# Performance work log

Hardware: AMD Instinct MI355X
Metric: run time of the kernel (lower is better)

Reference implementation:

```python
import jax, jax.numpy as jnp
import numpy as np

B, T, INPUT_DIM = 4, 2048, 1024
DIM, H = 64, 16  # per-head dim, n_heads


def setup_inputs() -> dict:
    key = jax.random.key(0)
    k1, k2, k3, k4 = jax.random.split(key, 4)
    x = jax.random.normal(k1, (B, T, INPUT_DIM), dtype=jnp.float32)
    # nn.Linear(input_dim, 3*h*d, bias=False)
    w_qkv = jax.random.normal(k2, (INPUT_DIM, 3 * H * DIM), dtype=jnp.float32) * (INPUT_DIM ** -0.5)
    # nn.Linear(h*d, input_dim) with bias
    w_out = jax.random.normal(k3, (H * DIM, INPUT_DIM), dtype=jnp.float32) * ((H * DIM) ** -0.5)
    b_out = jax.random.normal(k4, (INPUT_DIM,), dtype=jnp.float32) * 0.01
    return {"x": x, "w_qkv": w_qkv, "w_out": w_out, "b_out": b_out}


def reference(x, w_qkv, w_out, b_out):
    b, t, _ = x.shape
    scale = DIM ** -0.5
    qkv = x @ w_qkv                                   # [b, t, 3*h*d]
    # 'b t (qkv h d) -> qkv b h t d'
    qkv = qkv.reshape(b, t, 3, H, DIM)
    qkv = jnp.transpose(qkv, (2, 0, 3, 1, 4))         # [3, b, h, t, d]
    q, k, v = qkv[0], qkv[1], qkv[2]
    dot = jnp.einsum('bhtd,bhkd->bhtk', q, k) * scale # [b, h, t, t]
    att = jax.nn.softmax(dot, axis=-1)
    out = jnp.einsum('bhtk,bhkd->bhtd', att, v)       # [b, h, t, d]
    out = jnp.transpose(out, (0, 2, 1, 3)).reshape(b, t, H * DIM)
    return out @ w_out + b_out
```

## Files before the change

### kernel.cpp

```cpp
#include <hip/hip_runtime.h>
#include <hip/hip_bf16.h>
#include <stdint.h>

typedef __attribute__((ext_vector_type(8))) short bf16x8;
typedef __attribute__((ext_vector_type(4))) short s16x4;
typedef __attribute__((ext_vector_type(4))) float f32x4;

__device__ __forceinline__ void mfma_bf16(f32x4& c, bf16x8 a, bf16x8 b) {
  asm("v_mfma_f32_16x16x32_bf16 %0, %1, %2, %0" : "+v"(c) : "v"(a), "v"(b));
}

__device__ __forceinline__ void gload_lds16(const void* g, void* lds) {
  __builtin_amdgcn_global_load_lds(
      (const __attribute__((address_space(1))) void*)g,
      (__attribute__((address_space(3))) void*)lds, 16, 0, 0);
}

__global__ void cvt_f32_bf16(const float* __restrict__ in, __hip_bfloat16* __restrict__ out, int n4) {
  int i = blockIdx.x * blockDim.x + threadIdx.x;
  if (i >= n4) return;
  float4 v = reinterpret_cast<const float4*>(in)[i];
  __hip_bfloat162 a = __float22bfloat162_rn(make_float2(v.x, v.y));
  __hip_bfloat162 b = __float22bfloat162_rn(make_float2(v.z, v.w));
  reinterpret_cast<__hip_bfloat162*>(out)[i * 2]     = a;
  reinterpret_cast<__hip_bfloat162*>(out)[i * 2 + 1] = b;
}

__global__ void transpose_cvt(const float* __restrict__ in, __hip_bfloat16* __restrict__ out,
                              int R, int C) {
  __shared__ float tile[32][33];
  int c0 = blockIdx.x * 32, r0 = blockIdx.y * 32;
#pragma unroll
  for (int k = 0; k < 4; k++)
    tile[threadIdx.y + 8 * k][threadIdx.x] =
        in[(size_t)(r0 + threadIdx.y + 8 * k) * C + c0 + threadIdx.x];
  __syncthreads();
#pragma unroll
  for (int k = 0; k < 4; k++)
    out[(size_t)(c0 + threadIdx.y + 8 * k) * R + r0 + threadIdx.x] =
        __float2bfloat16(tile[threadIdx.x][threadIdx.y + 8 * k]);
}

template <int MODE>
__global__ __launch_bounds__(256) void gemm_bf16(
    const __hip_bfloat16* __restrict__ A, const __hip_bfloat16* __restrict__ Bt,
    int M, int N, int K,
    __hip_bfloat16* __restrict__ qb, __hip_bfloat16* __restrict__ kb,
    __hip_bfloat16* __restrict__ vt,
    float* __restrict__ outp, const float* __restrict__ bias) {
  constexpr int BK = 32;
  __shared__ __align__(16) __hip_bfloat16 As[128 * BK];
  __shared__ __align__(16) __hip_bfloat16 Bs[128 * BK];
  const int tid = threadIdx.x;
  const int wave = tid >> 6, lane = tid & 63;
  const int wr = wave >> 1, wc = wave & 1;
  const int m0 = blockIdx.y * 128;
  const int n0 = (MODE == 2 ? 2048 : 0) + blockIdx.x * 128;

  f32x4 acc[4][4];
#pragma unroll
  for (int i = 0; i < 4; i++)
#pragma unroll
    for (int j = 0; j < 4; j++) acc[i][j] = (f32x4)(0.0f);

  const int c0 = wave * 2, c1 = c0 + 1;
  const int srow0 = c0 * 16 + (lane >> 2);
  const int srow1 = c1 * 16 + (lane >> 2);
  const int scol = (lane & 3) * 8;
  const __hip_bfloat16* Ag0 = A + (size_t)(m0 + srow0) * K + scol;
  const __hip_bfloat16* Ag1 = A + (size_t)(m0 + srow1) * K + scol;
  const __hip_bfloat16* Bg0 = Bt + (size_t)(n0 + srow0) * K + scol;
  const __hip_bfloat16* Bg1 = Bt + (size_t)(n0 + srow1) * K + scol;
  __hip_bfloat16* AsP0 = &As[c0 * 512];
  __hip_bfloat16* AsP1 = &As[c1 * 512];
  __hip_bfloat16* BsP0 = &Bs[c0 * 512];
  __hip_bfloat16* BsP1 = &Bs[c1 * 512];

  for (int kk = 0; kk < K; kk += BK) {
    gload_lds16(Ag0 + kk, AsP0);
    gload_lds16(Ag1 + kk, AsP1);
    gload_lds16(Bg0 + kk, BsP0);
    gload_lds16(Bg1 + kk, BsP1);
    __syncthreads();
    bf16x8 af[4], bfr[4];
#pragma unroll
    for (int i = 0; i < 4; i++)
      af[i] = *(const bf16x8*)&As[(wr * 64 + i * 16 + (lane & 15)) * BK + (lane >> 4) * 8];
#pragma unroll
    for (int j = 0; j < 4; j++)
      bfr[j] = *(const bf16x8*)&Bs[(wc * 64 + j * 16 + (lane & 15)) * BK + (lane >> 4) * 8];
#pragma unroll
    for (int i = 0; i < 4; i++)
#pragma unroll
      for (int j = 0; j < 4; j++) {
        if constexpr (MODE == 2)
          mfma_bf16(acc[i][j], bfr[j], af[i]);
        else
          mfma_bf16(acc[i][j], af[i], bfr[j]);
      }
    __syncthreads();
  }

  if constexpr (MODE == 0) {
#pragma unroll
    for (int j = 0; j < 4; j++) {
      int col = n0 + wc * 64 + j * 16 + (lane & 15);
      int sel = col >> 10;
      int h = (col >> 6) & 15;
      int d = col & 63;
      __hip_bfloat16* dst = sel ? kb : qb;
      float scl = sel ? 1.0f : 0.18033688f;
#pragma unroll
      for (int i = 0; i < 4; i++) {
#pragma unroll
        for (int r = 0; r < 4; r++) {
          int row = m0 + wr * 64 + i * 16 + (lane >> 4) * 4 + r;
          int b = row >> 11, t = row & 2047;
          dst[(((size_t)b * 16 + h) * 2048 + t) * 64 + d] = __float2bfloat16(acc[i][j][r] * scl);
        }
      }
    }
  } else if constexpr (MODE == 2) {
#pragma unroll
    for (int j = 0; j < 4; j++) {
#pragma unroll
      for (int r = 0; r < 4; r++) {
        int nrow = n0 + wc * 64 + j * 16 + (lane >> 4) * 4 + r;
        int h = (nrow >> 6) & 15;
        int d = nrow & 63;
#pragma unroll
        for (int i = 0; i < 4; i++) {
          int tcol = m0 + wr * 64 + i * 16 + (lane & 15);
          int b = tcol >> 11, t = tcol & 2047;
          vt[(((size_t)b * 16 + h) * 64 + d) * 2048 + t] = __float2bfloat16(acc[i][j][r]);
        }
      }
    }
  } else {
#pragma unroll
    for (int j = 0; j < 4; j++) {
      int col = n0 + wc * 64 + j * 16 + (lane & 15);
      float bv = bias[col];
#pragma unroll
      for (int i = 0; i < 4; i++) {
#pragma unroll
        for (int r = 0; r < 4; r++) {
          int row = m0 + wr * 64 + i * 16 + (lane >> 4) * 4 + r;
          outp[(size_t)row * N + col] = acc[i][j][r] + bv;
        }
      }
    }
  }
}

__global__ __launch_bounds__(256) void attn_fwd(
    const __hip_bfloat16* __restrict__ Qb, const __hip_bfloat16* __restrict__ Kb,
    const __hip_bfloat16* __restrict__ Vtg, __hip_bfloat16* __restrict__ Ob) {
  constexpr int T = 2048;
  constexpr float THR = 11.5f;
  __shared__ __align__(16) __hip_bfloat16 Ks[2][4096];
  __shared__ __align__(16) __hip_bfloat16 Vs[2][4096];
  __shared__ __align__(16) __hip_bfloat16 Ps[4][1024];
  const int tid = threadIdx.x, wave = tid >> 6, lane = tid & 63;

  int id = ((int)blockIdx.x & 7) * 256 + ((int)blockIdx.x >> 3);
  const int bh = id >> 5, q0 = (id & 31) * 64;
  const size_t baseQ = (size_t)bh * T * 64;
  const size_t baseV = (size_t)bh * 64 * T;

  bf16x8 qf[2];
  {
    const int qrow = q0 + wave * 16 + (lane & 15);
#pragma unroll
    for (int ks = 0; ks < 2; ks++)
      qf[ks] = *(const bf16x8*)&Qb[baseQ + (size_t)qrow * 64 + ks * 32 + (lane >> 4) * 8];
  }

  float m_run = -3.0e38f;
  float l_part = 0.0f;
  f32x4 o[4];
#pragma unroll
  for (int fd = 0; fd < 4; fd++) o[fd] = (f32x4)(0.0f);

  const int sr = lane >> 3;
  const int q8 = (lane & 7) ^ sr;
  const char* KgB = (const char*)(Kb + baseQ);
  const char* VgB = (const char*)(Vtg + baseV);
  const int cc0 = wave * 2, cc1 = cc0 + 1;
  char* PwB = (char*)&Ps[wave][0];
  const int prow = lane & 15, hi = lane >> 4;

#define STAGE(kt, buf)                                                                   \
  do {                                                                                   \
    char* kd = (char*)Ks[buf];                                                           \
    char* vd = (char*)Vs[buf];                                                           \
    gload_lds16(KgB + (size_t)((kt) * 64 + cc0 * 8 + sr) * 128 + q8 * 16, kd + cc0 * 1024); \
    gload_lds16(KgB + (size_t)((kt) * 64 + cc1 * 8 + sr) * 128 + q8 * 16, kd + cc1 * 1024); \
    gload_lds16(VgB + (size_t)(cc0 * 8 + sr) * 4096 + (kt) * 128 + q8 * 16, vd + cc0 * 1024); \
    gload_lds16(VgB + (size_t)(cc1 * 8 + sr) * 4096 + (kt) * 128 + q8 * 16, vd + cc1 * 1024); \
  } while (0)

  STAGE(0, 0);
  int cur = 0;

  for (int kt = 0; kt < T / 64; kt++) {
    if (kt < T / 64 - 1) {
      STAGE(kt + 1, cur ^ 1);
      asm volatile("s_waitcnt vmcnt(4)" ::: "memory");
    } else {
      asm volatile("s_waitcnt vmcnt(0)" ::: "memory");
    }
    __builtin_amdgcn_s_barrier();
    __builtin_amdgcn_sched_barrier(0);
    const char* KsB = (const char*)Ks[cur];
    const char* VtB = (const char*)Vs[cur];

    f32x4 s[4];
#pragma unroll
    for (int kf = 0; kf < 4; kf++) s[kf] = (f32x4)(0.0f);
    __builtin_amdgcn_s_setprio(1);
#pragma unroll
    for (int ks = 0; ks < 2; ks++) {
#pragma unroll
      for (int kf = 0; kf < 4; kf++) {
        int key = kf * 16 + prow;
        int byteoff = (key * 128 + ks * 64 + hi * 16) ^ ((key & 7) << 4);
        bf16x8 kfrag = *(const bf16x8*)(KsB + byteoff);
        mfma_bf16(s[kf], kfrag, qf[ks]);
      }
    }
    __builtin_amdgcn_s_setprio(0);

    float t0 = fmaxf(fmaxf(s[0][0], s[0][1]), s[0][2]);
    float t1 = fmaxf(fmaxf(s[0][3], s[1][0]), s[1][1]);
    float t2 = fmaxf(fmaxf(s[1][2], s[1][3]), s[2][0]);
    float t3 = fmaxf(fmaxf(s[2][1], s[2][2]), s[2][3]);
    float t4 = fmaxf(fmaxf(s[3][0], s[3][1]), s[3][2]);
    float tm = fmaxf(fmaxf(fmaxf(t0, t1), t2), fmaxf(fmaxf(t3, t4), s[3][3]));
    tm = fmaxf(tm, __shfl_xor(tm, 16));
    tm = fmaxf(tm, __shfl_xor(tm, 32));

    if (!__all(tm - m_run <= THR)) {
      float mn = fmaxf(m_run, tm);
      float alpha = __builtin_exp2f(m_run - mn);
      m_run = mn;
      l_part *= alpha;
#pragma unroll
      for (int r = 0; r < 4; r++) {
        float ar = __shfl(alpha, hi * 4 + r);
#pragma unroll
        for (int fd = 0; fd < 4; fd++) o[fd][r] *= ar;
      }
    }

    float rs0 = 0.0f, rs1 = 0.0f;
#pragma unroll
    for (int kf = 0; kf < 4; kf++) {
      float p0 = __builtin_exp2f(s[kf][0] - m_run);
      float p1 = __builtin_exp2f(s[kf][1] - m_run);
      float p2 = __builtin_exp2f(s[kf][2] - m_run);
      float p3 = __builtin_exp2f(s[kf][3] - m_run);
      rs0 += p0 + p1;
      rs1 += p2 + p3;
      __hip_bfloat162 h01 = __float22bfloat162_rn(make_float2(p0, p1));
      __hip_bfloat162 h23 = __float22bfloat162_rn(make_float2(p2, p3));
      int2 w;
      w.x = *(int*)&h01;
      w.y = *(int*)&h23;
      int wb = (prow * 128 + kf * 32 + hi * 8) ^ ((prow & 7) << 4);
      *(int2*)(PwB + wb) = w;
    }
    l_part += rs0 + rs1;

    __builtin_amdgcn_s_setprio(1);
#pragma unroll
    for (int ks = 0; ks < 2; ks++) {
      int pbyte = (prow * 128 + ks * 64 + hi * 16) ^ ((prow & 7) << 4);
      bf16x8 pa = *(const bf16x8*)(PwB + pbyte);
#pragma unroll
      for (int fd = 0; fd < 4; fd++) {
        int d = fd * 16 + prow;
        int vbyte = (d * 128 + ks * 64 + hi * 16) ^ ((d & 7) << 4);
        bf16x8 vf = *(const bf16x8*)(VtB + vbyte);
        mfma_bf16(o[fd], pa, vf);
      }
    }
    __builtin_amdgcn_s_setprio(0);
    __builtin_amdgcn_sched_barrier(0);
    __builtin_amdgcn_s_barrier();
    cur ^= 1;
  }
#undef STAGE

  float l_run = l_part;
  l_run += __shfl_xor(l_run, 16);
  l_run += __shfl_xor(l_run, 32);
  const int b = bh >> 4, h = bh & 15;
#pragma unroll
  for (int r = 0; r < 4; r++) {
    float lr = __shfl(l_run, hi * 4 + r);
    float inv = 1.0f / lr;
    int trow = q0 + wave * 16 + hi * 4 + r;
#pragma unroll
    for (int fd = 0; fd < 4; fd++) {
      int col = h * 64 + fd * 16 + prow;
      Ob[((size_t)(b * 2048 + trow)) * 1024 + col] = __float2bfloat16(o[fd][r] * inv);
    }
  }
}

extern "C" void kernel_launch(void* const* d_in, const int* in_sizes, int n_in,
                              void* d_out, int out_size, void* d_ws, size_t ws_size,
                              hipStream_t stream) {
  const float* x = (const float*)d_in[0];
  const float* w_qkv = (const float*)d_in[1];
  const float* w_out = (const float*)d_in[2];
  const float* b_out = (const float*)d_in[3];
  float* out = (float*)d_out;

  size_t need = (size_t)37748736 * 2;
  if (ws_size < need) return;
  __hip_bfloat16* wsp = (__hip_bfloat16*)d_ws;
  __hip_bfloat16* x_bf = wsp;
  __hip_bfloat16* wqkv_t = x_bf + 8192 * 1024;
  __hip_bfloat16* wout_t = wqkv_t + 3072 * 1024;
  __hip_bfloat16* qb = wout_t + 1024 * 1024;
  __hip_bfloat16* kb = qb + 8388608;
  __hip_bfloat16* vt = kb + 8388608;
  __hip_bfloat16* ab = x_bf;

  cvt_f32_bf16<<<8192, 256, 0, stream>>>(x, x_bf, 8192 * 1024 / 4);
  transpose_cvt<<<dim3(3072 / 32, 1024 / 32), dim3(32, 8), 0, stream>>>(w_qkv, wqkv_t, 1024, 3072);
  transpose_cvt<<<dim3(1024 / 32, 1024 / 32), dim3(32, 8), 0, stream>>>(w_out, wout_t, 1024, 1024);
  gemm_bf16<0><<<dim3(16, 64), 256, 0, stream>>>(x_bf, wqkv_t, 8192, 3072, 1024,
                                                 qb, kb, nullptr, nullptr, nullptr);
  gemm_bf16<2><<<dim3(8, 64), 256, 0, stream>>>(x_bf, wqkv_t, 8192, 3072, 1024,
                                                nullptr, nullptr, vt, nullptr, nullptr);
  attn_fwd<<<2048, 256, 0, stream>>>(qb, kb, vt, ab);
  gemm_bf16<1><<<dim3(8, 64), 256, 0, stream>>>(ab, wout_t, 8192, 1024, 1024,
                                                nullptr, nullptr, nullptr, out, b_out);
}
```

Baseline: 249.6 us.

## Use 32x32 MFMA in attention with register-resident P via permlane swaps

Rewrites the attention kernel to use 32x32x16 bf16 MFMA tiles, so each wave owns 32 query rows and each block covers 128 queries, halving the grid. The softmax probabilities stay in registers and are rearranged into the B-operand layout with v_permlane32_swap instead of being written to and read back from LDS. This is meant to double K/V tile reuse per block, remove the P staging traffic, and simplify the row-max and rescale shuffles. The trade-offs are more accumulator registers per wave, which may lower occupancy, and fewer blocks to spread across the CUs.

```diff
diff --git a/kernel.cpp b/kernel.cpp
--- a/kernel.cpp
+++ b/kernel.cpp
@@ -5,9 +5,13 @@
 typedef __attribute__((ext_vector_type(8))) short bf16x8;
 typedef __attribute__((ext_vector_type(4))) short s16x4;
 typedef __attribute__((ext_vector_type(4))) float f32x4;
+typedef __attribute__((ext_vector_type(16))) float f32x16;
 
 __device__ __forceinline__ void mfma_bf16(f32x4& c, bf16x8 a, bf16x8 b) {
   asm("v_mfma_f32_16x16x32_bf16 %0, %1, %2, %0" : "+v"(c) : "v"(a), "v"(b));
+}
+__device__ __forceinline__ void mfma32_bf16(f32x16& c, bf16x8 a, bf16x8 b) {
+  asm("v_mfma_f32_32x32x16_bf16 %0, %1, %2, %0" : "+v"(c) : "v"(a), "v"(b));
 }
 
 __device__ __forceinline__ void gload_lds16(const void* g, void* lds) {
@@ -160,42 +164,37 @@
   constexpr float THR = 11.5f;
   __shared__ __align__(16) __hip_bfloat16 Ks[2][4096];
   __shared__ __align__(16) __hip_bfloat16 Vs[2][4096];
-  __shared__ __align__(16) __hip_bfloat16 Ps[4][1024];
   const int tid = threadIdx.x, wave = tid >> 6, lane = tid & 63;
 
-  int id = ((int)blockIdx.x & 7) * 256 + ((int)blockIdx.x >> 3);
-  const int bh = id >> 5, q0 = (id & 31) * 64;
+  int id = ((int)blockIdx.x & 7) * 128 + ((int)blockIdx.x >> 3);
+  const int bh = id >> 4, q0 = (id & 15) * 128;
   const size_t baseQ = (size_t)bh * T * 64;
   const size_t baseV = (size_t)bh * 64 * T;
-
-  bf16x8 qf[2];
-  {
-    const int qrow = q0 + wave * 16 + (lane & 15);
-#pragma unroll
-    for (int ks = 0; ks < 2; ks++)
-      qf[ks] = *(const bf16x8*)&Qb[baseQ + (size_t)qrow * 64 + ks * 32 + (lane >> 4) * 8];
-  }
+  const int l31 = lane & 31, half = lane >> 5;
+
+  bf16x8 qf[4];
+  const int qrow = q0 + wave * 32 + l31;
+#pragma unroll
+  for (int ks = 0; ks < 4; ks++)
+    qf[ks] = *(const bf16x8*)&Qb[baseQ + (size_t)qrow * 64 + ks * 16 + half * 8];
 
   float m_run = -3.0e38f;
   float l_part = 0.0f;
-  f32x4 o[4];
-#pragma unroll
-  for (int fd = 0; fd < 4; fd++) o[fd] = (f32x4)(0.0f);
+  f32x16 o0 = (f32x16)(0.0f), o1 = (f32x16)(0.0f);
 
   const int sr = lane >> 3;
   const int q8 = (lane & 7) ^ sr;
   const char* KgB = (const char*)(Kb + baseQ);
   const char* VgB = (const char*)(Vtg + baseV);
   const int cc0 = wave * 2, cc1 = cc0 + 1;
-  char* PwB = (char*)&Ps[wave][0];
-  const int prow = lane & 15, hi = lane >> 4;
-
-#define STAGE(kt, buf)                                                                   \
-  do {                                                                                   \
-    char* kd = (char*)Ks[buf];                                                           \
-    char* vd = (char*)Vs[buf];                                                           \
-    gload_lds16(KgB + (size_t)((kt) * 64 + cc0 * 8 + sr) * 128 + q8 * 16, kd + cc0 * 1024); \
-    gload_lds16(KgB + (size_t)((kt) * 64 + cc1 * 8 + sr) * 128 + q8 * 16, kd + cc1 * 1024); \
+  const int swz = (l31 & 7) << 4;
+
+#define STAGE(kt, buf)                                                                        \
+  do {                                                                                        \
+    char* kd = (char*)Ks[buf];                                                                \
+    char* vd = (char*)Vs[buf];                                                                \
+    gload_lds16(KgB + (size_t)((kt) * 64 + cc0 * 8 + sr) * 128 + q8 * 16, kd + cc0 * 1024);   \
+    gload_lds16(KgB + (size_t)((kt) * 64 + cc1 * 8 + sr) * 128 + q8 * 16, kd + cc1 * 1024);   \
     gload_lds16(VgB + (size_t)(cc0 * 8 + sr) * 4096 + (kt) * 128 + q8 * 16, vd + cc0 * 1024); \
     gload_lds16(VgB + (size_t)(cc1 * 8 + sr) * 4096 + (kt) * 128 + q8 * 16, vd + cc1 * 1024); \
   } while (0)
@@ -215,29 +214,23 @@
     const char* KsB = (const char*)Ks[cur];
     const char* VtB = (const char*)Vs[cur];
 
-    f32x4 s[4];
-#pragma unroll
-    for (int kf = 0; kf < 4; kf++) s[kf] = (f32x4)(0.0f);
+    f32x16 s0 = (f32x16)(0.0f), s1 = (f32x16)(0.0f);
     __builtin_amdgcn_s_setprio(1);
 #pragma unroll
-    for (int ks = 0; ks < 2; ks++) {
-#pragma unroll
-      for (int kf = 0; kf < 4; kf++) {
-        int key = kf * 16 + prow;
-        int byteoff = (key * 128 + ks * 64 + hi * 16) ^ ((key & 7) << 4);
-        bf16x8 kfrag = *(const bf16x8*)(KsB + byteoff);
-        mfma_bf16(s[kf], kfrag, qf[ks]);
-      }
+    for (int ks = 0; ks < 4; ks++) {
+      bf16x8 kf0 = *(const bf16x8*)(KsB + ((l31 * 128 + ks * 32 + half * 16) ^ swz));
+      bf16x8 kf1 = *(const bf16x8*)(KsB + (((32 + l31) * 128 + ks * 32 + half * 16) ^ swz));
+      mfma32_bf16(s0, kf0, qf[ks]);
+      mfma32_bf16(s1, kf1, qf[ks]);
     }
     __builtin_amdgcn_s_setprio(0);
 
-    float t0 = fmaxf(fmaxf(s[0][0], s[0][1]), s[0][2]);
-    float t1 = fmaxf(fmaxf(s[0][3], s[1][0]), s[1][1]);
-    float t2 = fmaxf(fmaxf(s[1][2], s[1][3]), s[2][0]);
-    float t3 = fmaxf(fmaxf(s[2][1], s[2][2]), s[2][3]);
-    float t4 = fmaxf(fmaxf(s[3][0], s[3][1]), s[3][2]);
-    float tm = fmaxf(fmaxf(fmaxf(t0, t1), t2), fmaxf(fmaxf(t3, t4), s[3][3]));
-    tm = fmaxf(tm, __shfl_xor(tm, 16));
+    float mx[8];
+#pragma unroll
+    for (int i = 0; i < 8; i++)
+      mx[i] = fmaxf(fmaxf(s0[2 * i], s0[2 * i + 1]), fmaxf(s1[2 * i], s1[2 * i + 1]));
+    float tm = fmaxf(fmaxf(fmaxf(mx[0], mx[1]), fmaxf(mx[2], mx[3])),
+                     fmaxf(fmaxf(mx[4], mx[5]), fmaxf(mx[6], mx[7])));
     tm = fmaxf(tm, __shfl_xor(tm, 32));
 
     if (!__all(tm - m_run <= THR)) {
@@ -246,44 +239,49 @@
       m_run = mn;
       l_part *= alpha;
 #pragma unroll
-      for (int r = 0; r < 4; r++) {
-        float ar = __shfl(alpha, hi * 4 + r);
-#pragma unroll
-        for (int fd = 0; fd < 4; fd++) o[fd][r] *= ar;
+      for (int r = 0; r < 16; r++) {
+        o0[r] *= alpha;
+        o1[r] *= alpha;
       }
     }
 
     float rs0 = 0.0f, rs1 = 0.0f;
 #pragma unroll
-    for (int kf = 0; kf < 4; kf++) {
-      float p0 = __builtin_exp2f(s[kf][0] - m_run);
-      float p1 = __builtin_exp2f(s[kf][1] - m_run);
-      float p2 = __builtin_exp2f(s[kf][2] - m_run);
-      float p3 = __builtin_exp2f(s[kf][3] - m_run);
-      rs0 += p0 + p1;
-      rs1 += p2 + p3;
-      __hip_bfloat162 h01 = __float22bfloat162_rn(make_float2(p0, p1));
-      __hip_bfloat162 h23 = __float22bfloat162_rn(make_float2(p2, p3));
-      int2 w;
-      w.x = *(int*)&h01;
-      w.y = *(int*)&h23;
-      int wb = (prow * 128 + kf * 32 + hi * 8) ^ ((prow & 7) << 4);
-      *(int2*)(PwB + wb) = w;
+    for (int r = 0; r < 16; r++) {
+      s0[r] = __builtin_exp2f(s0[r] - m_run);
+      s1[r] = __builtin_exp2f(s1[r] - m_run);
+      rs0 += s0[r];
+      rs1 += s1[r];
     }
     l_part += rs0 + rs1;
 
     __builtin_amdgcn_s_setprio(1);
 #pragma unroll
-    for (int ks = 0; ks < 2; ks++) {
-      int pbyte = (prow * 128 + ks * 64 + hi * 16) ^ ((prow & 7) << 4);
-      bf16x8 pa = *(const bf16x8*)(PwB + pbyte);
-#pragma unroll
-      for (int fd = 0; fd < 4; fd++) {
-        int d = fd * 16 + prow;
-        int vbyte = (d * 128 + ks * 64 + hi * 16) ^ ((d & 7) << 4);
-        bf16x8 vf = *(const bf16x8*)(VtB + vbyte);
-        mfma_bf16(o[fd], pa, vf);
-      }
+    for (int kb = 0; kb < 2; kb++) {
+      int cw[8];
+#pragma unroll
+      for (int m = 0; m < 8; m++) {
+        float pa = (kb == 0) ? s0[2 * m] : s1[2 * m];
+        float pb = (kb == 0) ? s0[2 * m + 1] : s1[2 * m + 1];
+        __hip_bfloat162 h2 = __float22bfloat162_rn(make_float2(pa, pb));
+        cw[m] = *(int*)&h2;
+      }
+      asm("v_permlane32_swap_b32 %0, %1" : "+v"(cw[0]), "+v"(cw[2]));
+      asm("v_permlane32_swap_b32 %0, %1" : "+v"(cw[1]), "+v"(cw[3]));
+      asm("v_permlane32_swap_b32 %0, %1" : "+v"(cw[4]), "+v"(cw[6]));
+      asm("v_permlane32_swap_b32 %0, %1" : "+v"(cw[5]), "+v"(cw[7]));
+      int4 w0 = make_int4(cw[0], cw[1], cw[2], cw[3]);
+      int4 w1 = make_int4(cw[4], cw[5], cw[6], cw[7]);
+      bf16x8 pb0 = *(bf16x8*)&w0;
+      bf16x8 pb1 = *(bf16x8*)&w1;
+      bf16x8 va0 = *(const bf16x8*)(VtB + ((l31 * 128 + kb * 64 + half * 16) ^ swz));
+      bf16x8 vb0 = *(const bf16x8*)(VtB + (((32 + l31) * 128 + kb * 64 + half * 16) ^ swz));
+      bf16x8 va1 = *(const bf16x8*)(VtB + ((l31 * 128 + kb * 64 + 32 + half * 16) ^ swz));
+      bf16x8 vb1 = *(const bf16x8*)(VtB + (((32 + l31) * 128 + kb * 64 + 32 + half * 16) ^ swz));
+      mfma32_bf16(o0, va0, pb0);
+      mfma32_bf16(o1, vb0, pb0);
+      mfma32_bf16(o0, va1, pb1);
+      mfma32_bf16(o1, vb1, pb1);
     }
     __builtin_amdgcn_s_setprio(0);
     __builtin_amdgcn_sched_barrier(0);
@@ -292,19 +290,23 @@
   }
 #undef STAGE
 
-  float l_run = l_part;
-  l_run += __shfl_xor(l_run, 16);
-  l_run += __shfl_xor(l_run, 32);
+  float l_run = l_part + __shfl_xor(l_part, 32);
+  float inv = 1.0f / l_run;
   const int b = bh >> 4, h = bh & 15;
-#pragma unroll
-  for (int r = 0; r < 4; r++) {
-    float lr = __shfl(l_run, hi * 4 + r);
-    float inv = 1.0f / lr;
-    int trow = q0 + wave * 16 + hi * 4 + r;
-#pragma unroll
-    for (int fd = 0; fd < 4; fd++) {
-      int col = h * 64 + fd * 16 + prow;
-      Ob[((size_t)(b * 2048 + trow)) * 1024 + col] = __float2bfloat16(o[fd][r] * inv);
+  const int trow = q0 + wave * 32 + l31;
+  __hip_bfloat16* orow = Ob + ((size_t)(b * 2048 + trow)) * 1024 + h * 64;
+#pragma unroll
+  for (int db = 0; db < 2; db++) {
+#pragma unroll
+    for (int rq = 0; rq < 4; rq++) {
+      int d0 = db * 32 + rq * 8 + half * 4;
+      s16x4 w;
+#pragma unroll
+      for (int e = 0; e < 4; e++) {
+        float val = (db == 0 ? o0[rq * 4 + e] : o1[rq * 4 + e]) * inv;
+        w[e] = (short)__bfloat16_as_short(__float2bfloat16(val));
+      }
+      *(s16x4*)(orow + d0) = w;
     }
   }
 }
@@ -336,7 +338,7 @@
                                                  qb, kb, nullptr, nullptr, nullptr);
   gemm_bf16<2><<<dim3(8, 64), 256, 0, stream>>>(x_bf, wqkv_t, 8192, 3072, 1024,
                                                 nullptr, nullptr, vt, nullptr, nullptr);
-  attn_fwd<<<2048, 256, 0, stream>>>(qb, kb, vt, ab);
+  attn_fwd<<<1024, 256, 0, stream>>>(qb, kb, vt, ab);
   gemm_bf16<1><<<dim3(8, 64), 256, 0, stream>>>(ab, wout_t, 8192, 1024, 1024,
                                                 nullptr, nullptr, nullptr, out, b_out);
 }
```

New measurement: 248.5 us. No clear change (-0.5%).
